# Kernel optimization log

Hardware: AMD Instinct MI355X
Metric: run time of the kernel (lower is better)

The kernel has to match this reference:

```python
import jax, jax.numpy as jnp
import numpy as np
import math

HEADS = 16
D_MODEL = 1024
D_K = D_MODEL // HEADS
PRUNE_KEEP = 0.9  # code sets pruning_ratio=0.1 then flips to 1-0.1


def setup_inputs() -> dict:
    key = jax.random.key(0)
    ks = jax.random.split(key, 12)
    B, S = 2, 2048
    sc = 0.02
    return {
        "q": jax.random.normal(ks[0], (B, S, D_MODEL), jnp.float32),
        "k": jax.random.normal(ks[1], (B, S, D_MODEL), jnp.float32),
        "v": jax.random.normal(ks[2], (B, S, D_MODEL), jnp.float32),
        "Wq": jax.random.normal(ks[3], (D_MODEL, D_MODEL), jnp.float32) * sc,
        "bq": jnp.zeros((D_MODEL,), jnp.float32),
        "Wk": jax.random.normal(ks[4], (D_MODEL, D_MODEL), jnp.float32) * sc,
        "bk": jnp.zeros((D_MODEL,), jnp.float32),
        "Wv": jax.random.normal(ks[5], (D_MODEL, D_MODEL), jnp.float32) * sc,
        "bv": jnp.zeros((D_MODEL,), jnp.float32),
        "Wo": jax.random.normal(ks[6], (D_MODEL, D_MODEL), jnp.float32) * sc,
        "bo": jnp.zeros((D_MODEL,), jnp.float32),
    }


def _split_heads(x, B):
    # [B, S, D] -> [B, H, S, d_k]
    return x.reshape(B, -1, HEADS, D_K).transpose(0, 2, 1, 3)


def _pruned_attention(q, k, v):
    # q,k,v: [B,H,S,d_k]
    B, H, S, _ = q.shape
    scores = jnp.einsum("bhqd,bhkd->bhqk", q, k) / math.sqrt(D_K)
    scores = jax.nn.softmax(scores, axis=-1)  # [B,H,S,S]
    keep = int(S * PRUNE_KEEP)
    col_sum = jnp.sum(scores, axis=2)  # [B,H,S] (sum over query dim)
    _, idx = jax.lax.top_k(col_sum, keep)  # [B,H,keep]
    mask = jnp.zeros((B, H, S), scores.dtype).at[
        jnp.arange(B)[:, None, None], jnp.arange(H)[None, :, None], idx
    ].set(1.0)
    pruned = scores * mask[:, :, None, :]
    # dropout in eval = identity, so the pruned scores feed AV
    return jnp.einsum("bhqk,bhkd->bhqd", pruned, v)


def reference(q, k, v, Wq, bq, Wk, bk, Wv, bv, Wo, bo):
    B = q.shape[0]
    qh = _split_heads(q @ Wq.T + bq, B)
    kh = _split_heads(k @ Wk.T + bk, B)
    vh = _split_heads(v @ Wv.T + bv, B)
    out = _pruned_attention(qh, kh, vh)  # [B,H,S,d_k]
    concat = out.transpose(0, 2, 1, 3).reshape(B, -1, D_MODEL)
    return concat @ Wo.T + bo
```

## Files before the change

kernel.cpp:

```cpp
#include <hip/hip_runtime.h>


typedef __attribute__((ext_vector_type(8))) short short8;
typedef __attribute__((ext_vector_type(4))) short short4v;
typedef __attribute__((ext_vector_type(4))) float f32x4;
typedef __attribute__((ext_vector_type(16))) float f32x16;
typedef __attribute__((ext_vector_type(4))) unsigned int u32x4;

#define KEEP 1843

#if __has_builtin(__builtin_amdgcn_exp2f)
  #define PEXP(x) __builtin_amdgcn_exp2f(x)
  #define QSC 0.18033688011112042f
#else
  #define PEXP(x) __expf(x)
  #define QSC 0.125f
#endif

#define AS1(p) ((const __attribute__((address_space(1))) void*)(p))
#define AS3(p) ((__attribute__((address_space(3))) void*)(p))

static __device__ __forceinline__ float bf2f(unsigned short s) {
    union { unsigned u; float f; } v; v.u = ((unsigned)s) << 16; return v.f;
}
static __device__ __forceinline__ unsigned short f2bf(float f) {
    union { float f; unsigned u; } v; v.f = f;
    unsigned u = v.u;
    unsigned r = (u + 0x7FFFu + ((u >> 16) & 1u)) >> 16;
    return (unsigned short)r;
}

#define MFMA(A, B, C)   __builtin_amdgcn_mfma_f32_16x16x32_bf16(A, B, C, 0, 0, 0)
#define MFMA32(A, B, C) __builtin_amdgcn_mfma_f32_32x32x16_bf16(A, B, C, 0, 0, 0)


__global__ __launch_bounds__(256) void cvt_all(
    const float* __restrict__ q,  const float* __restrict__ k,
    const float* __restrict__ v,  const float* __restrict__ Wq,
    const float* __restrict__ Wk, const float* __restrict__ Wv,
    const float* __restrict__ Wo,
    unsigned short* __restrict__ qh, unsigned short* __restrict__ ql,
    unsigned short* __restrict__ kh, unsigned short* __restrict__ kl,
    unsigned short* __restrict__ vh,
    unsigned short* __restrict__ wqh, unsigned short* __restrict__ wql,
    unsigned short* __restrict__ wkh, unsigned short* __restrict__ wkl,
    unsigned short* __restrict__ wvh,
    unsigned short* __restrict__ woh, unsigned short* __restrict__ wol,
    float* __restrict__ zbuf)
{
    int g = blockIdx.x * 256 + threadIdx.x;
    if (g >= 4194304) {
        int idx = g - 4194304;
        ((f32x4*)zbuf)[idx] = (f32x4){0.f, 0.f, 0.f, 0.f};
        return;
    }
    const float* in; unsigned short* oh; unsigned short* ol; int idx;
    if (g < 3145728) {
        int seg = g >> 20; idx = g & 1048575;
        if (seg == 0)      { in = q; oh = qh;  ol = ql;  }
        else if (seg == 1) { in = k; oh = kh;  ol = kl;  }
        else               { in = v; oh = vh;  ol = 0;   }
    } else {
        int gw = g - 3145728; int seg = gw >> 18; idx = gw & 262143;
        if (seg == 0)      { in = Wq; oh = wqh; ol = wql; }
        else if (seg == 1) { in = Wk; oh = wkh; ol = wkl; }
        else if (seg == 2) { in = Wv; oh = wvh; ol = 0;   }
        else               { in = Wo; oh = woh; ol = wol; }
    }
    f32x4 x = ((const f32x4*)in)[idx];
    short4v h, l;
#pragma unroll
    for (int j = 0; j < 4; j++) {
        unsigned short hv = f2bf(x[j]);
        h[j] = (short)hv;
        l[j] = (short)f2bf(x[j] - bf2f(hv));
    }
    ((short4v*)oh)[idx] = h;
    if (ol) ((short4v*)ol)[idx] = l;
}

__global__ __launch_bounds__(256) void gemm_qkv(
    const short* __restrict__ A0, const short* __restrict__ Al0,
    const short* __restrict__ A1, const short* __restrict__ Al1,
    const short* __restrict__ W0, const short* __restrict__ Wl0,
    const short* __restrict__ W1, const short* __restrict__ Wl1,
    const float* __restrict__ b0, const float* __restrict__ b1,
    unsigned short* __restrict__ Qhi, unsigned short* __restrict__ Qlo,
    unsigned short* __restrict__ Khi, unsigned short* __restrict__ Klo)
{
    int lin = blockIdx.x + (blockIdx.y << 3) + (blockIdx.z << 8);
    int tile = (lin & 7) * 64 + (lin >> 3);
    int bx = tile & 7, by = (tile >> 3) & 31, bz = tile >> 8;

    const short *Ahg, *Alg, *Whg, *Wlg; const float* bias;
    unsigned short *oh, *ol; float scale;
    if (bz == 0) { Ahg=A0; Alg=Al0; Whg=W0; Wlg=Wl0; bias=b0; oh=Qhi; ol=Qlo; scale=QSC;  }
    else         { Ahg=A1; Alg=Al1; Whg=W1; Wlg=Wl1; bias=b1; oh=Khi; ol=Klo; scale=1.0f; }

    __shared__ __align__(16) short Ah_l[128*32];
    __shared__ __align__(16) short Al_l[128*32];
    __shared__ __align__(16) short Wh_l[128*32];
    __shared__ __align__(16) short Wl_l[128*32];

    int tid  = threadIdx.x;
    int w    = tid >> 6;
    int lane = tid & 63;
    int ln   = lane & 15;
    int quad = lane >> 4;
    int rowBase = by * 128;
    int colBase = bx * 128;
    int mBase = (w & 1) * 64;
    int nBase = (w >> 1) * 64;

    int srow = (lane >> 2);
    int scol = (((lane & 3) ^ ((lane >> 3) & 3))) * 8;
    int cs = ((quad ^ ((ln >> 1) & 3))) * 8;

    const short* Ag_h = Ahg + (size_t)rowBase * 1024;
    const short* Ag_l = Alg + (size_t)rowBase * 1024;
    const short* Wg_h = Whg + (size_t)colBase * 1024;
    const short* Wg_l = Wlg + (size_t)colBase * 1024;

    f32x4 acc[4][4];
#pragma unroll
    for (int i = 0; i < 4; i++)
#pragma unroll
        for (int j = 0; j < 4; j++) acc[i][j] = (f32x4){0.f, 0.f, 0.f, 0.f};

    for (int kk = 0; kk < 1024; kk += 32) {
#pragma unroll
        for (int j = 0; j < 2; j++) {
            int r = w*32 + j*16;
            size_t go = (size_t)(r + srow) * 1024 + kk + scol;
            __builtin_amdgcn_global_load_lds(AS1(Ag_h + go), AS3(Ah_l + r*32), 16, 0, 0);
            __builtin_amdgcn_global_load_lds(AS1(Ag_l + go), AS3(Al_l + r*32), 16, 0, 0);
            __builtin_amdgcn_global_load_lds(AS1(Wg_h + go), AS3(Wh_l + r*32), 16, 0, 0);
            __builtin_amdgcn_global_load_lds(AS1(Wg_l + go), AS3(Wl_l + r*32), 16, 0, 0);
        }
        __syncthreads();

        short8 ah[4], al[4], bh[4], bl[4];
#pragma unroll
        for (int mt = 0; mt < 4; mt++) {
            int r = mBase + mt*16 + ln;
            ah[mt] = *(const short8*)(Ah_l + r*32 + cs);
            al[mt] = *(const short8*)(Al_l + r*32 + cs);
        }
#pragma unroll
        for (int nt = 0; nt < 4; nt++) {
            int c = nBase + nt*16 + ln;
            bh[nt] = *(const short8*)(Wh_l + c*32 + cs);
            bl[nt] = *(const short8*)(Wl_l + c*32 + cs);
        }
#pragma unroll
        for (int mt = 0; mt < 4; mt++)
#pragma unroll
            for (int nt = 0; nt < 4; nt++) {
                acc[mt][nt] = MFMA(ah[mt], bh[nt], acc[mt][nt]);
                acc[mt][nt] = MFMA(ah[mt], bl[nt], acc[mt][nt]);
                acc[mt][nt] = MFMA(al[mt], bh[nt], acc[mt][nt]);
            }
        __syncthreads();
    }

#pragma unroll
    for (int mt = 0; mt < 4; mt++) {
#pragma unroll
        for (int nt = 0; nt < 4; nt++) {
            int col = colBase + nBase + nt*16 + ln;
            float bv = bias[col];
#pragma unroll
            for (int i = 0; i < 4; i++) {
                int row = rowBase + mBase + mt*16 + quad*4 + i;
                float val = (acc[mt][nt][i] + bv) * scale;
                int b_  = row >> 11, s = row & 2047;
                int h   = col >> 6,  d = col & 63;
                int bh_ = b_ * 16 + h;
                size_t idx = (size_t)bh_ * 131072 + (size_t)(s >> 5) * 2048
                    + ((size_t)(((d >> 4) * 2 + ((d >> 3) & 1)) * 32 + (s & 31))) * 8 + (d & 7);
                unsigned short hv = f2bf(val);
                oh[idx] = hv;
                ol[idx] = f2bf(val - bf2f(hv));
            }
        }
    }
}

__global__ __launch_bounds__(256) void gemm_v(
    const short* __restrict__ Ag, const short* __restrict__ Whg,
    const float* __restrict__ bias, const float* __restrict__ maskf,
    unsigned short* __restrict__ Vt)
{
    int lin = blockIdx.x + (blockIdx.y << 4);
    int tile = (lin & 7) * 64 + (lin >> 3);
    int bx = tile & 15, by = tile >> 4;

    __shared__ __align__(16) short A_l[128*32];
    __shared__ __align__(16) short Wh_l[64*32];

    int tid  = threadIdx.x;
    int w    = tid >> 6;
    int lane = tid & 63;
    int ln   = lane & 15;
    int quad = lane >> 4;
    int rowBase = by * 128;
    int colBase = bx * 64;
    int mBase = (w & 1) * 64;
    int nBase = (w >> 1) * 32;

    int srow = (lane >> 2);
    int scol = (((lane & 3) ^ ((lane >> 3) & 3))) * 8;
    int cs = ((quad ^ ((ln >> 1) & 3))) * 8;
    const short* Abase = Ag  + (size_t)rowBase * 1024;
    const short* Whb   = Whg + (size_t)colBase * 1024;

    f32x4 acc[4][2];
#pragma unroll
    for (int i = 0; i < 4; i++)
#pragma unroll
        for (int j = 0; j < 2; j++) acc[i][j] = (f32x4){0.f, 0.f, 0.f, 0.f};

    for (int kk = 0; kk < 1024; kk += 32) {
#pragma unroll
        for (int j = 0; j < 2; j++) {
            int r = w*32 + j*16;
            size_t go = (size_t)(r + srow) * 1024 + kk + scol;
            __builtin_amdgcn_global_load_lds(AS1(Abase + go), AS3(A_l + r*32), 16, 0, 0);
        }
        {
            int c = w * 16;
            size_t go = (size_t)(c + srow) * 1024 + kk + scol;
            __builtin_amdgcn_global_load_lds(AS1(Whb + go), AS3(Wh_l + c*32), 16, 0, 0);
        }
        __syncthreads();

        short8 a[4], bh2[2];
#pragma unroll
        for (int mt = 0; mt < 4; mt++)
            a[mt] = *(const short8*)(A_l + (mBase + mt*16 + ln)*32 + cs);
#pragma unroll
        for (int nt = 0; nt < 2; nt++)
            bh2[nt] = *(const short8*)(Wh_l + (nBase + nt*16 + ln)*32 + cs);
#pragma unroll
        for (int mt = 0; mt < 4; mt++)
#pragma unroll
            for (int nt = 0; nt < 2; nt++)
                acc[mt][nt] = MFMA(a[mt], bh2[nt], acc[mt][nt]);
        __syncthreads();
    }

#pragma unroll
    for (int mt = 0; mt < 4; mt++) {
#pragma unroll
        for (int nt = 0; nt < 2; nt++) {
            int col = colBase + nBase + nt*16 + ln;
            float bv = bias[col];
#pragma unroll
            for (int i = 0; i < 4; i++) {
                int row = rowBase + mBase + mt*16 + quad*4 + i;
                float val = acc[mt][nt][i] + bv;
                int b_  = row >> 11, s = row & 2047;
                int h   = col >> 6,  d = col & 63;
                int bh_ = b_ * 16 + h;
                val *= maskf[bh_ * 2048 + s];
                size_t idx = (size_t)bh_ * 131072 + (size_t)(s >> 5) * 2048
                    + ((size_t)((((((s >> 4) & 1) * 2 + (d >> 5)) * 2 + ((s >> 3) & 1)) * 32)
                                + (d & 31))) * 8 + (s & 7);
                Vt[idx] = f2bf(val);
            }
        }
    }
}

__global__ __launch_bounds__(256) void gemm_out(
    const short* __restrict__ Ag, const short* __restrict__ Whg,
    const short* __restrict__ Wlg, const float* __restrict__ bias,
    float* __restrict__ out)
{
    int lin = blockIdx.x + (blockIdx.y << 4);
    int tile = (lin & 7) * 64 + (lin >> 3);
    int bx = tile & 15, by = tile >> 4;

    __shared__ __align__(16) short A_l[128*32];
    __shared__ __align__(16) short Wh_l[64*32];
    __shared__ __align__(16) short Wl_l[64*32];

    int tid  = threadIdx.x;
    int w    = tid >> 6;
    int lane = tid & 63;
    int ln   = lane & 15;
    int quad = lane >> 4;
    int rowBase = by * 128;
    int colBase = bx * 64;
    int mBase = (w & 1) * 64;
    int nBase = (w >> 1) * 32;

    int srow = (lane >> 2);
    int scol = (((lane & 3) ^ ((lane >> 3) & 3))) * 8;
    int cs = ((quad ^ ((ln >> 1) & 3))) * 8;
    const short* Abase = Ag  + (size_t)rowBase * 1024;
    const short* Whb   = Whg + (size_t)colBase * 1024;
    const short* Wlb   = Wlg + (size_t)colBase * 1024;

    f32x4 acc[4][2];
#pragma unroll
    for (int i = 0; i < 4; i++)
#pragma unroll
        for (int j = 0; j < 2; j++) acc[i][j] = (f32x4){0.f, 0.f, 0.f, 0.f};

    for (int kk = 0; kk < 1024; kk += 32) {
#pragma unroll
        for (int j = 0; j < 2; j++) {
            int r = w*32 + j*16;
            size_t go = (size_t)(r + srow) * 1024 + kk + scol;
            __builtin_amdgcn_global_load_lds(AS1(Abase + go), AS3(A_l + r*32), 16, 0, 0);
        }
        {
            int c = w * 16;
            size_t go = (size_t)(c + srow) * 1024 + kk + scol;
            __builtin_amdgcn_global_load_lds(AS1(Whb + go), AS3(Wh_l + c*32), 16, 0, 0);
            __builtin_amdgcn_global_load_lds(AS1(Wlb + go), AS3(Wl_l + c*32), 16, 0, 0);
        }
        __syncthreads();

        short8 a[4], bh2[2], bl2[2];
#pragma unroll
        for (int mt = 0; mt < 4; mt++)
            a[mt] = *(const short8*)(A_l + (mBase + mt*16 + ln)*32 + cs);
#pragma unroll
        for (int nt = 0; nt < 2; nt++) {
            int c = nBase + nt*16 + ln;
            bh2[nt] = *(const short8*)(Wh_l + c*32 + cs);
            bl2[nt] = *(const short8*)(Wl_l + c*32 + cs);
        }
#pragma unroll
        for (int mt = 0; mt < 4; mt++)
#pragma unroll
            for (int nt = 0; nt < 2; nt++) {
                acc[mt][nt] = MFMA(a[mt], bh2[nt], acc[mt][nt]);
                acc[mt][nt] = MFMA(a[mt], bl2[nt], acc[mt][nt]);
            }
        __syncthreads();
    }

#pragma unroll
    for (int mt = 0; mt < 4; mt++) {
#pragma unroll
        for (int nt = 0; nt < 2; nt++) {
            int col = colBase + nBase + nt*16 + ln;
            float bv = bias[col];
#pragma unroll
            for (int i = 0; i < 4; i++) {
                int row = rowBase + mBase + mt*16 + quad*4 + i;
                out[(size_t)row * 1024 + col] = acc[mt][nt][i] + bv;
            }
        }
    }
}

__global__ __launch_bounds__(256) void attn_rowsum(
    const short* __restrict__ Qhi, const short* __restrict__ Khi,
    float* __restrict__ rowsum)
{
    int bh = blockIdx.z, tid = threadIdx.x;
    int w = tid >> 6, lane = tid & 63, ln = lane & 15, quad = lane >> 4;
    int qb  = blockIdx.x * 256 + w * 64;
    int kt0 = blockIdx.y * 32;
    const short* QH = Qhi + (size_t)bh * 131072;
    const short* KH = Khi + (size_t)bh * 131072;

    short8 qh[4][2];
#pragma unroll
    for (int mt = 0; mt < 4; mt++)
#pragma unroll
        for (int half = 0; half < 2; half++) {
            size_t o = (size_t)((qb >> 5) + (mt >> 1)) * 2048
                     + (size_t)(half * 4 + quad) * 256 + ((mt & 1) * 16 + ln) * 8;
            qh[mt][half] = *(const short8*)(QH + o);
        }

    short8 kh[2][2];
    auto loadK = [&](int buf, int kt) {
        size_t ko = (size_t)(kt >> 1) * 2048 + (size_t)quad * 256 + ((kt & 1) * 16 + ln) * 8;
        kh[buf][0] = *(const short8*)(KH + ko);
        kh[buf][1] = *(const short8*)(KH + ko + 1024);
    };

    float racc[4][4] = {};
    auto comp = [&](int buf) {
#pragma unroll
        for (int mt = 0; mt < 4; mt++) {
            f32x4 c1 = (f32x4){0.f,0.f,0.f,0.f};
            c1 = MFMA(qh[mt][0], kh[buf][0], c1);
            c1 = MFMA(qh[mt][1], kh[buf][1], c1);
#pragma unroll
            for (int i = 0; i < 4; i++)
                racc[mt][i] += PEXP(c1[i]);
        }
    };

    loadK(0, kt0);
    for (int t = 0; t < 32; t += 2) {
        loadK(1, kt0 + t + 1);
        comp(0);
        if (t + 2 < 32) loadK(0, kt0 + t + 2);
        comp(1);
    }
#pragma unroll
    for (int mt = 0; mt < 4; mt++)
#pragma unroll
        for (int i = 0; i < 4; i++)
            for (int d = 1; d < 16; d <<= 1)
                racc[mt][i] += __shfl_xor(racc[mt][i], d, 64);
    if (ln == 0) {
#pragma unroll
        for (int mt = 0; mt < 4; mt++)
#pragma unroll
            for (int i = 0; i < 4; i++)
                atomicAdd(&rowsum[bh * 2048 + qb + mt*16 + quad*4 + i], racc[mt][i]);
    }
}

__global__ __launch_bounds__(256) void attn_colsum(
    const short* __restrict__ Qhi, const short* __restrict__ Qlo,
    const short* __restrict__ Khi, const short* __restrict__ Klo,
    const float* __restrict__ rowsum, float* __restrict__ colsum)
{
    __shared__ float sli[512];
    int bh = blockIdx.z, tid = threadIdx.x;
    int q0 = blockIdx.y * 512;
    for (int j = tid; j < 512; j += 256)
        sli[j] = 1.0f / rowsum[bh * 2048 + q0 + j];
    __syncthreads();

    int w = tid >> 6, lane = tid & 63, ln = lane & 15, quad = lane >> 4;
    int kb  = blockIdx.x * 256 + w * 64;
    int qt0 = blockIdx.y * 32;
    const short* QH = Qhi + (size_t)bh * 131072;
    const short* QL = Qlo + (size_t)bh * 131072;
    const short* KH = Khi + (size_t)bh * 131072;
    const short* KL = Klo + (size_t)bh * 131072;

    short8 kh[4][2], kl[4][2];
#pragma unroll
    for (int nt = 0; nt < 4; nt++)
#pragma unroll
        for (int half = 0; half < 2; half++) {
            size_t o = (size_t)((kb >> 5) + (nt >> 1)) * 2048 + (size_t)half * 1024
                     + (size_t)quad * 256 + ((nt & 1) * 16 + ln) * 8;
            kh[nt][half] = *(const short8*)(KH + o);
            kl[nt][half] = *(const short8*)(KL + o);
        }

    short8 qh[2][2], ql[2][2];
    auto loadQ = [&](int buf, int qt) {
        int qtt = qt0 + qt;
        size_t base = (size_t)(qtt >> 1) * 2048 + ((qtt & 1) * 16 + ln) * 8;
        qh[buf][0] = *(const short8*)(QH + base + (size_t)quad * 256);
        qh[buf][1] = *(const short8*)(QH + base + (size_t)(4 + quad) * 256);
        ql[buf][0] = *(const short8*)(QL + base + (size_t)quad * 256);
        ql[buf][1] = *(const short8*)(QL + base + (size_t)(4 + quad) * 256);
    };

    float cacc[4] = {0.f, 0.f, 0.f, 0.f};
    auto comp = [&](int buf, int qt) {
#pragma unroll
        for (int nt = 0; nt < 4; nt++) {
            f32x4 c1 = (f32x4){0.f,0.f,0.f,0.f};
            f32x4 c2 = (f32x4){0.f,0.f,0.f,0.f};
            c1 = MFMA(qh[buf][0], kh[nt][0], c1); c1 = MFMA(qh[buf][1], kh[nt][1], c1);
            c2 = MFMA(qh[buf][0], kl[nt][0], c2); c2 = MFMA(qh[buf][1], kl[nt][1], c2);
            c2 = MFMA(ql[buf][0], kh[nt][0], c2); c2 = MFMA(ql[buf][1], kh[nt][1], c2);
#pragma unroll
            for (int i = 0; i < 4; i++) {
                int r = qt*16 + quad*4 + i;
                cacc[nt] += PEXP(c1[i] + c2[i]) * sli[r];
            }
        }
    };

    loadQ(0, 0);
    for (int qt = 0; qt < 32; qt += 2) {
        loadQ(1, qt + 1);
        comp(0, qt);
        if (qt + 2 < 32) loadQ(0, qt + 2);
        comp(1, qt + 1);
    }
#pragma unroll
    for (int nt = 0; nt < 4; nt++) {
        cacc[nt] += __shfl_xor(cacc[nt], 16, 64);
        cacc[nt] += __shfl_xor(cacc[nt], 32, 64);
        if (lane < 16) atomicAdd(&colsum[bh * 2048 + kb + nt*16 + lane], cacc[nt]);
    }
}

__global__ __launch_bounds__(256) void topk_mask(
    const float* __restrict__ colsum, float* __restrict__ maskf)
{
    __shared__ unsigned keys[2048];
    __shared__ int hist[256];
    __shared__ unsigned sh_pref;
    __shared__ int sh_need;
    int bh = blockIdx.x, tid = threadIdx.x;
    for (int j = tid; j < 2048; j += 256) {
        unsigned u = __float_as_uint(colsum[bh * 2048 + j]);
        keys[j] = (u & 0x80000000u) ? ~u : (u | 0x80000000u);
    }
    if (tid == 0) { sh_pref = 0; sh_need = KEEP; }
    __syncthreads();
#pragma unroll
    for (int shift = 24; shift >= 0; shift -= 8) {
        hist[tid & 255] = 0;
        __syncthreads();
        unsigned pref = sh_pref;
        unsigned hmask = (shift == 24) ? 0u : (0xFFFFFFFFu << (shift + 8));
        for (int j = tid; j < 2048; j += 256) {
            unsigned ky = keys[j];
            if ((ky & hmask) == pref)
                atomicAdd(&hist[(ky >> shift) & 255], 1);
        }
        __syncthreads();
        if (tid == 0) {
            int need = sh_need, acc = 0, d = 255;
            for (; d >= 0; d--) {
                if (acc + hist[d] >= need) break;
                acc += hist[d];
            }
            sh_pref = pref | ((unsigned)d << shift);
            sh_need = need - acc;
        }
        __syncthreads();
    }
    unsigned thr = sh_pref;
    for (int j = tid; j < 2048; j += 256)
        maskf[bh * 2048 + j] = (keys[j] >= thr) ? 1.0f : 0.0f;
}

__global__ __launch_bounds__(256) void attn_av(
    const short* __restrict__ Qhi, const short* __restrict__ Kf,
    const short* __restrict__ Vf, const float* __restrict__ rowsum,
    unsigned short* __restrict__ concat)
{
    __shared__ __align__(16) short KA[4096];
    __shared__ __align__(16) short KB[4096];
    int lin = blockIdx.x + (blockIdx.y << 4);
    int tile = (lin & 7) * 64 + (lin >> 3);
    int bxx = tile & 15, bh = tile >> 4;
    int tid = threadIdx.x;
    int w = tid >> 6, lane = tid & 63;
    int lq = lane & 31, hi = lane >> 5;
    int qb = bxx * 128 + w * 32;
    const short* Qb = Qhi + (size_t)bh * 131072 + (size_t)(qb >> 5) * 2048;
    const short* Kg = Kf  + (size_t)bh * 131072;
    const short* Vg = Vf  + (size_t)bh * 131072;

    short8 qf[4];
#pragma unroll
    for (int d = 0; d < 4; d++)
        qf[d] = *(const short8*)(Qb + (size_t)(d*2 + hi) * 256 + lq * 8);

    f32x16 o0, o1;
#pragma unroll
    for (int i = 0; i < 16; i++) { o0[i] = 0.f; o1[i] = 0.f; }

    auto STAGE = [&](short* B, int kc) {
        __builtin_amdgcn_global_load_lds(AS1(Kg + (size_t)kc*2048 + tid*8),
                                         AS3(B + w*512), 16, 0, 0);
        __builtin_amdgcn_global_load_lds(AS1(Vg + (size_t)kc*2048 + tid*8),
                                         AS3(B + 2048 + w*512), 16, 0, 0);
    };

    auto comp = [&](const short* B) {
        short8 kf_[4], vf_[4];
#pragma unroll
        for (int d = 0; d < 4; d++)
            kf_[d] = *(const short8*)(B + (d*2 + hi)*256 + lq*8);
#pragma unroll
        for (int ks = 0; ks < 2; ks++)
#pragma unroll
            for (int nt = 0; nt < 2; nt++)
                vf_[ks*2+nt] = *(const short8*)(B + 2048 + ((ks*2+nt)*2 + hi)*256 + lq*8);

        f32x16 s;
#pragma unroll
        for (int i = 0; i < 16; i++) s[i] = 0.f;
        s = MFMA32(kf_[0], qf[0], s);
        s = MFMA32(kf_[1], qf[1], s);
        s = MFMA32(kf_[2], qf[2], s);
        s = MFMA32(kf_[3], qf[3], s);

        float p[16];
#pragma unroll
        for (int i = 0; i < 16; i++) p[i] = PEXP(s[i]);

        short8 pa[2];
#pragma unroll
        for (int ks = 0; ks < 2; ks++) {
            unsigned w0, w1, w2, w3;
            int o8 = ks * 8;
            asm("v_cvt_pk_bf16_f32 %0, %1, %2" : "=v"(w0) : "v"(p[o8+0]), "v"(p[o8+1]));
            asm("v_cvt_pk_bf16_f32 %0, %1, %2" : "=v"(w1) : "v"(p[o8+2]), "v"(p[o8+3]));
            asm("v_cvt_pk_bf16_f32 %0, %1, %2" : "=v"(w2) : "v"(p[o8+4]), "v"(p[o8+5]));
            asm("v_cvt_pk_bf16_f32 %0, %1, %2" : "=v"(w3) : "v"(p[o8+6]), "v"(p[o8+7]));
            asm("v_permlane32_swap_b32 %0, %1" : "+v"(w0), "+v"(w2));
            asm("v_permlane32_swap_b32 %0, %1" : "+v"(w1), "+v"(w3));
            u32x4 pw = { w0, w1, w2, w3 };
            pa[ks] = __builtin_bit_cast(short8, pw);
        }

        o0 = MFMA32(pa[0], vf_[0], o0);
        o1 = MFMA32(pa[0], vf_[1], o1);
        o0 = MFMA32(pa[1], vf_[2], o0);
        o1 = MFMA32(pa[1], vf_[3], o1);
    };

    STAGE(KA, 0);
    __syncthreads();
    for (int kc = 0; kc < 64; kc += 2) {
        STAGE(KB, kc + 1);
        comp(KA);
        __syncthreads();
        if (kc + 2 < 64) STAGE(KA, kc + 2);
        comp(KB);
        __syncthreads();
    }

    int b_ = bh >> 4, h = bh & 15;
#pragma unroll
    for (int r = 0; r < 16; r++) {
        int crow = (r & 3) + 8*(r >> 2) + 4*hi;
        float inv = 1.0f / rowsum[bh * 2048 + qb + crow];
        size_t base = ((size_t)(b_*2048 + qb + crow)) * 1024 + h*64;
        concat[base + lq]      = f2bf(o0[r] * inv);
        concat[base + 32 + lq] = f2bf(o1[r] * inv);
    }
}

extern "C" void kernel_launch(void* const* d_in, const int* in_sizes, int n_in,
                              void* d_out, int out_size, void* d_ws, size_t ws_size,
                              hipStream_t stream)
{
    const float* q  = (const float*)d_in[0];
    const float* k  = (const float*)d_in[1];
    const float* v  = (const float*)d_in[2];
    const float* Wq = (const float*)d_in[3];
    const float* bq = (const float*)d_in[4];
    const float* Wk = (const float*)d_in[5];
    const float* bk = (const float*)d_in[6];
    const float* Wv = (const float*)d_in[7];
    const float* bv = (const float*)d_in[8];
    const float* Wo = (const float*)d_in[9];
    const float* bo = (const float*)d_in[10];

    char* ws = (char*)d_ws;
    size_t off = 0;
    auto alloc = [&](size_t bytes) -> void* {
        void* p = ws + off;
        off += (bytes + 255) & ~(size_t)255;
        return p;
    };
    const size_t ASZ = (size_t)4096 * 1024 * 2;
    const size_t WSZ = (size_t)1024 * 1024 * 2;
    unsigned short* qh_ = (unsigned short*)alloc(ASZ);
    unsigned short* ql_ = (unsigned short*)alloc(ASZ);
    unsigned short* kh_ = (unsigned short*)alloc(ASZ);
    unsigned short* kl_ = (unsigned short*)alloc(ASZ);
    unsigned short* vh_ = (unsigned short*)alloc(ASZ);
    unsigned short* wqh = (unsigned short*)alloc(WSZ);
    unsigned short* wql = (unsigned short*)alloc(WSZ);
    unsigned short* wkh = (unsigned short*)alloc(WSZ);
    unsigned short* wkl = (unsigned short*)alloc(WSZ);
    unsigned short* wvh = (unsigned short*)alloc(WSZ);
    unsigned short* woh = (unsigned short*)alloc(WSZ);
    unsigned short* wol = (unsigned short*)alloc(WSZ);
    short* Qhi = (short*)alloc(ASZ);
    short* Qlo = (short*)alloc(ASZ);
    short* Khi = (short*)alloc(ASZ);
    short* Klo = (short*)alloc(ASZ);
    short* Vt  = (short*)alloc(ASZ);
    float* rowsum = (float*)alloc((size_t)32 * 2048 * 4);
    float* colsum = (float*)alloc((size_t)32 * 2048 * 4);
    float* maskf  = (float*)alloc((size_t)32 * 2048 * 4);
    unsigned short* concat = (unsigned short*)alloc(ASZ);

    dim3 blk(256);

    cvt_all<<<dim3(16512), blk, 0, stream>>>(
        q, k, v, Wq, Wk, Wv, Wo,
        qh_, ql_, kh_, kl_, vh_, wqh, wql, wkh, wkl, wvh, woh, wol,
        rowsum );

    gemm_qkv<<<dim3(8, 32, 2), blk, 0, stream>>>(
        (const short*)qh_, (const short*)ql_, (const short*)kh_, (const short*)kl_,
        (const short*)wqh, (const short*)wql, (const short*)wkh, (const short*)wkl,
        bq, bk,
        (unsigned short*)Qhi, (unsigned short*)Qlo,
        (unsigned short*)Khi, (unsigned short*)Klo);

    attn_rowsum<<<dim3(8, 4, 32), blk, 0, stream>>>(Qhi, Khi, rowsum);
    attn_colsum<<<dim3(8, 4, 32), blk, 0, stream>>>(Qhi, Qlo, Khi, Klo, rowsum, colsum);
    topk_mask  <<<dim3(32),   blk, 0, stream>>>(colsum, maskf);

    gemm_v<<<dim3(16, 32), blk, 0, stream>>>(
        (const short*)vh_, (const short*)wvh, bv, maskf, (unsigned short*)Vt);

    attn_av    <<<dim3(16, 32), blk, 0, stream>>>(Qhi, Khi, Vt, rowsum, concat);

    gemm_out<<<dim3(16, 32), blk, 0, stream>>>((const short*)concat,
        (const short*)woh, (const short*)wol, bo, (float*)d_out);
}
```

Measured before the change: 387.9 us.

## Double attn_av stage size and parallelize top-k digit selection with scan

The attention-AV kernel now stages two 32-key chunks of K and V per LDS buffer (64 keys per stage), halving the number of barriers and loop iterations. The top-k radix select replaces the serial single-thread digit search with a parallel suffix-sum scan across 256 threads. The larger LDS footprint (32KB per block) may reduce occupancy, and the scan adds 16 barriers per radix pass to the small topk kernel.

```diff
diff --git a/kernel.cpp b/kernel.cpp
--- a/kernel.cpp
+++ b/kernel.cpp
@@ -499,6 +499,7 @@
 {
     __shared__ unsigned keys[2048];
     __shared__ int hist[256];
+    __shared__ int suf[256];
     __shared__ unsigned sh_pref;
     __shared__ int sh_need;
     int bh = blockIdx.x, tid = threadIdx.x;
@@ -510,9 +511,10 @@
     __syncthreads();
 #pragma unroll
     for (int shift = 24; shift >= 0; shift -= 8) {
-        hist[tid & 255] = 0;
-        __syncthreads();
+        int need = sh_need;
         unsigned pref = sh_pref;
+        hist[tid] = 0;
+        __syncthreads();
         unsigned hmask = (shift == 24) ? 0u : (0xFFFFFFFFu << (shift + 8));
         for (int j = tid; j < 2048; j += 256) {
             unsigned ky = keys[j];
@@ -520,14 +522,18 @@
                 atomicAdd(&hist[(ky >> shift) & 255], 1);
         }
         __syncthreads();
-        if (tid == 0) {
-            int need = sh_need, acc = 0, d = 255;
-            for (; d >= 0; d--) {
-                if (acc + hist[d] >= need) break;
-                acc += hist[d];
-            }
-            sh_pref = pref | ((unsigned)d << shift);
-            sh_need = need - acc;
+        suf[tid] = hist[tid];
+        __syncthreads();
+#pragma unroll
+        for (int st = 1; st < 256; st <<= 1) {
+            int add = (tid + st < 256) ? suf[tid + st] : 0;
+            __syncthreads();
+            suf[tid] += add;
+            __syncthreads();
+        }
+        if (suf[tid] >= need && suf[tid] - hist[tid] < need) {
+            sh_pref = pref | ((unsigned)tid << shift);
+            sh_need = need - (suf[tid] - hist[tid]);
         }
         __syncthreads();
     }
@@ -541,8 +547,8 @@
     const short* __restrict__ Vf, const float* __restrict__ rowsum,
     unsigned short* __restrict__ concat)
 {
-    __shared__ __align__(16) short KA[4096];
-    __shared__ __align__(16) short KB[4096];
+    __shared__ __align__(16) short KA[8192];
+    __shared__ __align__(16) short KB[8192];
     int lin = blockIdx.x + (blockIdx.y << 4);
     int tile = (lin & 7) * 64 + (lin >> 3);
     int bxx = tile & 15, bh = tile >> 4;
@@ -563,23 +569,25 @@
 #pragma unroll
     for (int i = 0; i < 16; i++) { o0[i] = 0.f; o1[i] = 0.f; }
 
-    auto STAGE = [&](short* B, int kc) {
-        __builtin_amdgcn_global_load_lds(AS1(Kg + (size_t)kc*2048 + tid*8),
-                                         AS3(B + w*512), 16, 0, 0);
-        __builtin_amdgcn_global_load_lds(AS1(Vg + (size_t)kc*2048 + tid*8),
-                                         AS3(B + 2048 + w*512), 16, 0, 0);
+    auto STAGE = [&](short* B, int c) {
+        const short* Kc = Kg + (size_t)c * 4096;
+        const short* Vc = Vg + (size_t)c * 4096;
+        __builtin_amdgcn_global_load_lds(AS1(Kc + tid*8),        AS3(B + w*512), 16, 0, 0);
+        __builtin_amdgcn_global_load_lds(AS1(Kc + 2048 + tid*8), AS3(B + 2048 + w*512), 16, 0, 0);
+        __builtin_amdgcn_global_load_lds(AS1(Vc + tid*8),        AS3(B + 4096 + w*512), 16, 0, 0);
+        __builtin_amdgcn_global_load_lds(AS1(Vc + 2048 + tid*8), AS3(B + 4096 + 2048 + w*512), 16, 0, 0);
     };
 
-    auto comp = [&](const short* B) {
+    auto half_comp = [&](const short* Bk, const short* Bv) {
         short8 kf_[4], vf_[4];
 #pragma unroll
         for (int d = 0; d < 4; d++)
-            kf_[d] = *(const short8*)(B + (d*2 + hi)*256 + lq*8);
+            kf_[d] = *(const short8*)(Bk + (d*2 + hi)*256 + lq*8);
 #pragma unroll
         for (int ks = 0; ks < 2; ks++)
 #pragma unroll
             for (int nt = 0; nt < 2; nt++)
-                vf_[ks*2+nt] = *(const short8*)(B + 2048 + ((ks*2+nt)*2 + hi)*256 + lq*8);
+                vf_[ks*2+nt] = *(const short8*)(Bv + ((ks*2+nt)*2 + hi)*256 + lq*8);
 
         f32x16 s;
 #pragma unroll
@@ -613,14 +621,18 @@
         o0 = MFMA32(pa[1], vf_[2], o0);
         o1 = MFMA32(pa[1], vf_[3], o1);
     };
+    auto comp = [&](const short* B) {
+        half_comp(B, B + 4096);
+        half_comp(B + 2048, B + 4096 + 2048);
+    };
 
     STAGE(KA, 0);
     __syncthreads();
-    for (int kc = 0; kc < 64; kc += 2) {
-        STAGE(KB, kc + 1);
+    for (int c = 0; c < 32; c += 2) {
+        STAGE(KB, c + 1);
         comp(KA);
         __syncthreads();
-        if (kc + 2 < 64) STAGE(KA, kc + 2);
+        if (c + 2 < 32) STAGE(KA, c + 2);
         comp(KB);
         __syncthreads();
     }
```

Measured after the change: 350.7 us. -9.6%, faster.
